# Performance work log

Hardware: AMD Instinct MI355X
Metric: run time of the kernel (lower is better)

## Reference

```python
import jax, jax.numpy as jnp
import numpy as np

HIDDEN = 4096
NUM_EXPERTS = 64
TOP_K = 2
BATCH, SEQ = 4, 8192


def setup_inputs() -> dict:
    key = jax.random.key(0)
    kx, kw = jax.random.split(key)
    x = jax.random.normal(kx, (BATCH, SEQ, HIDDEN), dtype=jnp.float32)
    # nn.Linear default init ~ U(-1/sqrt(fan_in), 1/sqrt(fan_in)); scale ok for a gate
    bound = 1.0 / np.sqrt(HIDDEN)
    W = jax.random.uniform(kw, (NUM_EXPERTS, HIDDEN), dtype=jnp.float32,
                           minval=-bound, maxval=bound)
    return {"x": x, "W": W}


def reference(x, W):
    batch, seq_len, hidden = x.shape
    x_flat = x.reshape(-1, hidden)                       # [T, H]
    router_logits = jnp.einsum('th,eh->te', x_flat, W)   # [T, E] skinny GEMM
    probs = jax.nn.softmax(router_logits, axis=-1)       # [T, E]
    routing_weights, expert_indices = jax.lax.top_k(probs, TOP_K)  # [T, k]
    routing_weights = routing_weights / jnp.sum(routing_weights, axis=-1, keepdims=True)
    router_logits = router_logits.reshape(batch, seq_len, -1)
    return (router_logits, routing_weights, expert_indices)
```

## Files before the change

### kernel.cpp

```cpp
#include <hip/hip_runtime.h>
#include <math.h>

#define H 4096
#define E 64
#define T_TOTAL 32768
#define TB 64
#define NT 256
#define KC 64
#define NCH (H / KC)
#define OFF_W 2097152
#define OFF_I 2162688

#define AS1 __attribute__((address_space(1)))
#define AS3 __attribute__((address_space(3)))

#define GLD16(SRC, DST)                                                      \
  __builtin_amdgcn_global_load_lds((const AS1 void*)(SRC), (AS3 void*)(DST), \
                                   16, 0, 0)

__device__ __forceinline__ int swz(int row) { return (row ^ (row >> 4)) & 15; }

__global__ __launch_bounds__(NT, 2)
void moe_router_kernel(const float* __restrict__ x,
                       const float* __restrict__ W,
                       float* __restrict__ out)
{
    __shared__ float xt[2][TB * KC];
    __shared__ float wt[2][E * KC];

    const int tid  = threadIdx.x;
    const int tg   = tid & 15;
    const int eg   = tid >> 4;
    const int tok0 = blockIdx.x * TB;

    const float* xsrc[4];
    const float* wsrc[4];
    int dsto[4];
#pragma unroll
    for (int k = 0; k < 4; ++k) {
        const int u   = tid + k * NT;
        const int row = u >> 4;
        const int c4  = (u & 15) ^ swz(row);
        xsrc[k] = x + (size_t)(tok0 + row) * H + (c4 << 2);
        wsrc[k] = W + (size_t)row * H + (c4 << 2);
        dsto[k] = u * 4;
    }

    int xbase[4], wbase[4];
#pragma unroll
    for (int i = 0; i < 4; ++i) {
        const int xr = 4 * tg + i;
        const int wr = 4 * eg + i;
        xbase[i] = xr * KC + (swz(xr) << 2);
        wbase[i] = wr * KC + (swz(wr) << 2);
    }

    float acc[4][4];
#pragma unroll
    for (int i = 0; i < 4; ++i)
#pragma unroll
        for (int j = 0; j < 4; ++j) acc[i][j] = 0.f;

#pragma unroll
    for (int k = 0; k < 4; ++k) {
        GLD16(xsrc[k], &xt[0][dsto[k]]);
        GLD16(wsrc[k], &wt[0][dsto[k]]);
    }
    __syncthreads();

    for (int c = 0; c < NCH; ++c) {
        const int b = c & 1;

        if (c + 1 < NCH) {
#pragma unroll
            for (int k = 0; k < 4; ++k) {
                GLD16(xsrc[k] + (c + 1) * KC, &xt[b ^ 1][dsto[k]]);
                GLD16(wsrc[k] + (c + 1) * KC, &wt[b ^ 1][dsto[k]]);
            }
        }

        const float* xp = &xt[b][0];
        const float* wp = &wt[b][0];
#pragma unroll
        for (int s = 0; s < 16; ++s) {
            float4 xv[4], wv[4];
#pragma unroll
            for (int i = 0; i < 4; ++i)
                xv[i] = *(const float4*)(xp + (xbase[i] ^ (4 * s)));
#pragma unroll
            for (int j = 0; j < 4; ++j)
                wv[j] = *(const float4*)(wp + (wbase[j] ^ (4 * s)));
#pragma unroll
            for (int i = 0; i < 4; ++i)
#pragma unroll
                for (int j = 0; j < 4; ++j) {
                    acc[i][j] = fmaf(xv[i].x, wv[j].x, acc[i][j]);
                    acc[i][j] = fmaf(xv[i].y, wv[j].y, acc[i][j]);
                    acc[i][j] = fmaf(xv[i].z, wv[j].z, acc[i][j]);
                    acc[i][j] = fmaf(xv[i].w, wv[j].w, acc[i][j]);
                }
        }

        __syncthreads();
    }

#pragma unroll
    for (int i = 0; i < 4; ++i) {
        float4 v; v.x = acc[i][0]; v.y = acc[i][1]; v.z = acc[i][2]; v.w = acc[i][3];
        *(float4*)(out + (size_t)(tok0 + 4 * tg + i) * E + 4 * eg) = v;
    }

    float* lt = &xt[0][0];
#pragma unroll
    for (int i = 0; i < 4; ++i)
#pragma unroll
        for (int j = 0; j < 4; ++j)
            lt[(4 * tg + i) * 65 + 4 * eg + j] = acc[i][j];
    __syncthreads();

    if (tid < TB) {
        const float* row = lt + tid * 65;
        float v1 = -INFINITY, v2 = -INFINITY;
        int i1 = 0, i2 = 0;
        for (int e = 0; e < E; ++e) {
            float v = row[e];
            if (v > v1)      { v2 = v1; i2 = i1; v1 = v; i1 = e; }
            else if (v > v2) { v2 = v;  i2 = e; }
        }
        float ee = expf(v2 - v1);
        float w1 = 1.0f / (1.0f + ee);
        float w2 = ee * w1;

        const size_t tok = (size_t)tok0 + tid;
        out[OFF_W + tok * 2]     = w1;
        out[OFF_W + tok * 2 + 1] = w2;
        out[OFF_I + tok * 2]     = (float)i1;
        out[OFF_I + tok * 2 + 1] = (float)i2;
    }
}

extern "C" void kernel_launch(void* const* d_in, const int* in_sizes, int n_in,
                              void* d_out, int out_size, void* d_ws, size_t ws_size,
                              hipStream_t stream) {
    const float* x = (const float*)d_in[0];
    const float* W = (const float*)d_in[1];
    float* out = (float*)d_out;

    dim3 grid(T_TOTAL / TB);
    dim3 block(NT);
    moe_router_kernel<<<grid, block, 0, stream>>>(x, W, out);
}
```

Baseline: 376.2 us.

## Load W rows directly into registers per wave and double the token tile

```diff
diff --git a/kernel.cpp b/kernel.cpp
--- a/kernel.cpp
+++ b/kernel.cpp
@@ -4,8 +4,8 @@
 #define H 4096
 #define E 64
 #define T_TOTAL 32768
-#define TB 64
-#define NT 256
+#define TB 128
+#define NT 512
 #define KC 64
 #define NCH (H / KC)
 #define OFF_W 2097152
@@ -18,54 +18,76 @@
   __builtin_amdgcn_global_load_lds((const AS1 void*)(SRC), (AS3 void*)(DST), \
                                    16, 0, 0)
 
-__device__ __forceinline__ int swz(int row) { return (row ^ (row >> 4)) & 15; }
+__device__ __forceinline__ int swz(int r) { return (r ^ (r >> 4)) & 15; }
 
-__global__ __launch_bounds__(NT, 2)
+#define XSTEP(S, WC, WN, XC0, XC1, XN0, XN1)                                 \
+  do {                                                                       \
+    const int kn = ((S) == 15)                                               \
+                       ? ((c + 1 < NCH) ? (c + 1) * KC : c * KC)             \
+                       : c * KC + ((S) + 1) * 4;                             \
+    _Pragma("unroll")                                                        \
+    for (int j = 0; j < 8; ++j)                                              \
+      WN[j] = *(const float4*)(wbase + (size_t)j * H + kn);                  \
+    if ((S) < 15) {                                                          \
+      XN0 = *(const float4*)(xp + (xb0 ^ (((S) + 1) << 2)));                 \
+      XN1 = *(const float4*)(xp + (xb1 ^ (((S) + 1) << 2)));                 \
+    }                                                                        \
+    _Pragma("unroll")                                                        \
+    for (int j = 0; j < 8; ++j) {                                            \
+      acc0[j] = fmaf((XC0).x, WC[j].x, acc0[j]);                             \
+      acc0[j] = fmaf((XC0).y, WC[j].y, acc0[j]);                             \
+      acc0[j] = fmaf((XC0).z, WC[j].z, acc0[j]);                             \
+      acc0[j] = fmaf((XC0).w, WC[j].w, acc0[j]);                             \
+      acc1[j] = fmaf((XC1).x, WC[j].x, acc1[j]);                             \
+      acc1[j] = fmaf((XC1).y, WC[j].y, acc1[j]);                             \
+      acc1[j] = fmaf((XC1).z, WC[j].z, acc1[j]);                             \
+      acc1[j] = fmaf((XC1).w, WC[j].w, acc1[j]);                             \
+    }                                                                        \
+  } while (0)
+
+__global__ __launch_bounds__(NT, 1)
 void moe_router_kernel(const float* __restrict__ x,
                        const float* __restrict__ W,
                        float* __restrict__ out)
 {
     __shared__ float xt[2][TB * KC];
-    __shared__ float wt[2][E * KC];
 
     const int tid  = threadIdx.x;
-    const int tg   = tid & 15;
-    const int eg   = tid >> 4;
+    const int lane = tid & 63;
+    const int wid  = __builtin_amdgcn_readfirstlane(tid >> 6);
+    const int e0   = 8 * wid;
     const int tok0 = blockIdx.x * TB;
+    const int t0   = tok0 + lane;
+    const int t1   = t0 + 64;
+
+    const float* wbase = W + (size_t)e0 * H;
 
     const float* xsrc[4];
-    const float* wsrc[4];
-    int dsto[4];
+    int xdst[4];
 #pragma unroll
     for (int k = 0; k < 4; ++k) {
         const int u   = tid + k * NT;
         const int row = u >> 4;
         const int c4  = (u & 15) ^ swz(row);
         xsrc[k] = x + (size_t)(tok0 + row) * H + (c4 << 2);
-        wsrc[k] = W + (size_t)row * H + (c4 << 2);
-        dsto[k] = u * 4;
+        xdst[k] = u * 4;
     }
 
-    int xbase[4], wbase[4];
+    const int xb0 = lane * KC + (swz(lane) << 2);
+    const int xb1 = (lane + 64) * KC + (swz(lane + 64) << 2);
+
+    float acc0[8], acc1[8];
 #pragma unroll
-    for (int i = 0; i < 4; ++i) {
-        const int xr = 4 * tg + i;
-        const int wr = 4 * eg + i;
-        xbase[i] = xr * KC + (swz(xr) << 2);
-        wbase[i] = wr * KC + (swz(wr) << 2);
-    }
-
-    float acc[4][4];
-#pragma unroll
-    for (int i = 0; i < 4; ++i)
-#pragma unroll
-        for (int j = 0; j < 4; ++j) acc[i][j] = 0.f;
+    for (int j = 0; j < 8; ++j) { acc0[j] = 0.f; acc1[j] = 0.f; }
 
 #pragma unroll
-    for (int k = 0; k < 4; ++k) {
-        GLD16(xsrc[k], &xt[0][dsto[k]]);
-        GLD16(wsrc[k], &wt[0][dsto[k]]);
-    }
+    for (int k = 0; k < 4; ++k) GLD16(xsrc[k], &xt[0][xdst[k]]);
+
+    float4 wA[8], wB[8];
+#pragma unroll
+    for (int j = 0; j < 8; ++j)
+        wA[j] = *(const float4*)(wbase + (size_t)j * H);
+
     __syncthreads();
 
     for (int c = 0; c < NCH; ++c) {
@@ -73,49 +95,55 @@
 
         if (c + 1 < NCH) {
 #pragma unroll
-            for (int k = 0; k < 4; ++k) {
-                GLD16(xsrc[k] + (c + 1) * KC, &xt[b ^ 1][dsto[k]]);
-                GLD16(wsrc[k] + (c + 1) * KC, &wt[b ^ 1][dsto[k]]);
-            }
+            for (int k = 0; k < 4; ++k)
+                GLD16(xsrc[k] + (c + 1) * KC, &xt[b ^ 1][xdst[k]]);
         }
 
         const float* xp = &xt[b][0];
-        const float* wp = &wt[b][0];
-#pragma unroll
-        for (int s = 0; s < 16; ++s) {
-            float4 xv[4], wv[4];
-#pragma unroll
-            for (int i = 0; i < 4; ++i)
-                xv[i] = *(const float4*)(xp + (xbase[i] ^ (4 * s)));
-#pragma unroll
-            for (int j = 0; j < 4; ++j)
-                wv[j] = *(const float4*)(wp + (wbase[j] ^ (4 * s)));
-#pragma unroll
-            for (int i = 0; i < 4; ++i)
-#pragma unroll
-                for (int j = 0; j < 4; ++j) {
-                    acc[i][j] = fmaf(xv[i].x, wv[j].x, acc[i][j]);
-                    acc[i][j] = fmaf(xv[i].y, wv[j].y, acc[i][j]);
-                    acc[i][j] = fmaf(xv[i].z, wv[j].z, acc[i][j]);
-                    acc[i][j] = fmaf(xv[i].w, wv[j].w, acc[i][j]);
-                }
-        }
+        float4 xc0 = *(const float4*)(xp + xb0);
+        float4 xc1 = *(const float4*)(xp + xb1);
+        float4 xd0, xd1;
+
+        XSTEP(0,  wA, wB, xc0, xc1, xd0, xd1);
+        XSTEP(1,  wB, wA, xd0, xd1, xc0, xc1);
+        XSTEP(2,  wA, wB, xc0, xc1, xd0, xd1);
+        XSTEP(3,  wB, wA, xd0, xd1, xc0, xc1);
+        XSTEP(4,  wA, wB, xc0, xc1, xd0, xd1);
+        XSTEP(5,  wB, wA, xd0, xd1, xc0, xc1);
+        XSTEP(6,  wA, wB, xc0, xc1, xd0, xd1);
+        XSTEP(7,  wB, wA, xd0, xd1, xc0, xc1);
+        XSTEP(8,  wA, wB, xc0, xc1, xd0, xd1);
+        XSTEP(9,  wB, wA, xd0, xd1, xc0, xc1);
+        XSTEP(10, wA, wB, xc0, xc1, xd0, xd1);
+        XSTEP(11, wB, wA, xd0, xd1, xc0, xc1);
+        XSTEP(12, wA, wB, xc0, xc1, xd0, xd1);
+        XSTEP(13, wB, wA, xd0, xd1, xc0, xc1);
+        XSTEP(14, wA, wB, xc0, xc1, xd0, xd1);
+        XSTEP(15, wB, wA, xd0, xd1, xc0, xc1);
 
         __syncthreads();
     }
 
-#pragma unroll
-    for (int i = 0; i < 4; ++i) {
-        float4 v; v.x = acc[i][0]; v.y = acc[i][1]; v.z = acc[i][2]; v.w = acc[i][3];
-        *(float4*)(out + (size_t)(tok0 + 4 * tg + i) * E + 4 * eg) = v;
+    {
+        float* o0 = out + (size_t)t0 * E + e0;
+        float* o1 = out + (size_t)t1 * E + e0;
+        float4 v;
+        v.x = acc0[0]; v.y = acc0[1]; v.z = acc0[2]; v.w = acc0[3];
+        *(float4*)o0 = v;
+        v.x = acc0[4]; v.y = acc0[5]; v.z = acc0[6]; v.w = acc0[7];
+        *(float4*)(o0 + 4) = v;
+        v.x = acc1[0]; v.y = acc1[1]; v.z = acc1[2]; v.w = acc1[3];
+        *(float4*)o1 = v;
+        v.x = acc1[4]; v.y = acc1[5]; v.z = acc1[6]; v.w = acc1[7];
+        *(float4*)(o1 + 4) = v;
     }
 
     float* lt = &xt[0][0];
 #pragma unroll
-    for (int i = 0; i < 4; ++i)
-#pragma unroll
-        for (int j = 0; j < 4; ++j)
-            lt[(4 * tg + i) * 65 + 4 * eg + j] = acc[i][j];
+    for (int j = 0; j < 8; ++j) {
+        lt[lane * 65 + e0 + j]        = acc0[j];
+        lt[(lane + 64) * 65 + e0 + j] = acc1[j];
+    }
     __syncthreads();
 
     if (tid < TB) {
```

New measurement: 578.8 us. 1.54x slower.
